# Kernel optimization log

Measured on AMD Instinct MI355X. Metric: run time of the kernel, lower is better.

## Reference

```python
import jax, jax.numpy as jnp
import numpy as np

B, S, D = 1, 2048, 2048
H, KV, HD = 32, 8, 64          # heads, kv heads, head_dim
WINDOW = 1024                  # sliding window (left), causal
ROPE_THETA = 10000.0


def setup_inputs() -> dict:
    key = jax.random.key(0)
    ks = jax.random.split(key, 5)
    scale = 1.0 / np.sqrt(D)
    x = jax.random.normal(ks[0], (B, S, D), dtype=jnp.float32)
    wq = jax.random.normal(ks[1], (D, H * HD), dtype=jnp.float32) * scale
    wk = jax.random.normal(ks[2], (D, KV * HD), dtype=jnp.float32) * scale
    wv = jax.random.normal(ks[3], (D, KV * HD), dtype=jnp.float32) * scale
    wo = jax.random.normal(ks[4], (H * HD, D), dtype=jnp.float32) * scale
    # RoPE frequencies: freqs_cis = exp(i * t * theta^{-2j/hd}), stored as cos/sin
    inv_freq = 1.0 / (ROPE_THETA ** (np.arange(0, HD, 2, dtype=np.float32) / HD))  # [HD/2]
    t = np.arange(S, dtype=np.float32)
    ang = np.outer(t, inv_freq)  # [S, HD/2]
    freqs_cos = jnp.asarray(np.cos(ang), dtype=jnp.float32)
    freqs_sin = jnp.asarray(np.sin(ang), dtype=jnp.float32)
    return {"x": x, "wq": wq, "wk": wk, "wv": wv, "wo": wo,
            "freqs_cos": freqs_cos, "freqs_sin": freqs_sin}


def _apply_rope(t, cos, sin):
    # t: [B,S,h,HD]; pairs (t[...,2i], t[...,2i+1]) form complex numbers
    tr = t.reshape(*t.shape[:-1], HD // 2, 2)
    a, b = tr[..., 0], tr[..., 1]
    c = cos[None, :, None, :]  # [1,S,1,HD/2]
    s = sin[None, :, None, :]
    ra = a * c - b * s
    rb = a * s + b * c
    return jnp.stack([ra, rb], axis=-1).reshape(t.shape)


def reference(x, wq, wk, wv, wo, freqs_cos, freqs_sin):
    q = (x @ wq).reshape(B, S, H, HD)
    k = (x @ wk).reshape(B, S, KV, HD)
    v = (x @ wv).reshape(B, S, KV, HD)
    q = _apply_rope(q, freqs_cos, freqs_sin)
    k = _apply_rope(k, freqs_cos, freqs_sin)
    # GQA: repeat kv heads to match query heads
    k = jnp.repeat(k, H // KV, axis=2)  # [B,S,H,HD]
    v = jnp.repeat(v, H // KV, axis=2)
    scale = jnp.asarray(1.0 / np.sqrt(HD), dtype=x.dtype)
    scores = jnp.einsum('bqhd,bkhd->bhqk', q, k) * scale  # [B,H,S,S]
    i = jnp.arange(S)[:, None]
    j = jnp.arange(S)[None, :]
    allowed = (j <= i) & (j >= i - WINDOW)  # causal + sliding window
    scores = jnp.where(allowed[None, None], scores, jnp.asarray(-1e30, dtype=scores.dtype))
    attn = jax.nn.softmax(scores, axis=-1)
    out = jnp.einsum('bhqk,bkhd->bqhd', attn, v).reshape(B, S, H * HD)
    return out @ wo
```

## Files before the change

### kernel.cpp

```cpp
#include <hip/hip_runtime.h>
#include <stdint.h>

typedef __bf16 bf16_t;
typedef __bf16 bf16x8 __attribute__((ext_vector_type(8)));
typedef __bf16 bf16x4 __attribute__((ext_vector_type(4)));
typedef float floatx4 __attribute__((ext_vector_type(4)));

#define AS3(p) ((__attribute__((address_space(3))) void*)(p))
#define AS1(p) ((__attribute__((address_space(1))) void*)(void*)(p))

__global__ __launch_bounds__(256) void prep_k(const float* __restrict__ x,
                                              const float* __restrict__ wq,
                                              const float* __restrict__ wk,
                                              const float* __restrict__ wv,
                                              const float* __restrict__ wo,
                                              bf16_t* __restrict__ xb,
                                              bf16_t* __restrict__ wt) {
  __shared__ __align__(16) bf16_t T[64][68];
  const int b = blockIdx.x;
  const int t = threadIdx.x;
  if (b < 2048) {
    const int i = (b * 256 + t) * 8;
    floatx4 a = *(const floatx4*)&x[i];
    floatx4 c = *(const floatx4*)&x[i + 4];
    bf16x8 o;
#pragma unroll
    for (int j = 0; j < 4; ++j) { o[j] = (bf16_t)a[j]; o[4 + j] = (bf16_t)c[j]; }
    *(bf16x8*)&xb[i] = o;
    return;
  }
  int b2 = b - 2048;
  const float* src;
  int ncols, bx, by;
  bf16_t* dst;
  if (b2 < 1024) {
    src = wq; ncols = 2048; dst = wt; bx = b2 & 31; by = b2 >> 5;
  } else if (b2 < 1280) {
    const int i2 = b2 - 1024;
    src = wk; ncols = 512; dst = wt + (size_t)2048 * 2048; bx = i2 & 7; by = i2 >> 3;
  } else if (b2 < 1536) {
    const int i2 = b2 - 1280;
    src = wv; ncols = 512; dst = wt + (size_t)2560 * 2048; bx = i2 & 7; by = i2 >> 3;
  } else {
    const int i2 = b2 - 1536;
    src = wo; ncols = 2048; dst = wt + (size_t)3072 * 2048; bx = i2 & 31; by = i2 >> 5;
  }
  const int nt = bx * 64, kt = by * 64;
  const int r0 = t >> 4;
  const int c0 = (t & 15) << 2;
#pragma unroll
  for (int p = 0; p < 4; ++p) {
    const int row = p * 16 + r0;
    floatx4 v = *(const floatx4*)&src[(size_t)(kt + row) * ncols + nt + c0];
    bf16x4 bb;
#pragma unroll
    for (int i = 0; i < 4; ++i) bb[i] = (bf16_t)v[i];
    *(bf16x4*)&T[row][c0] = bb;
  }
  __syncthreads();
#pragma unroll
  for (int p = 0; p < 4; ++p) {
    const int n = p * 16 + r0;
    bf16x4 tmp;
#pragma unroll
    for (int i = 0; i < 4; ++i) tmp[i] = T[c0 + i][n];
    *(bf16x4*)&dst[(size_t)(nt + n) * 2048 + kt + c0] = tmp;
  }
}

template <int EPI>
__global__ __launch_bounds__(256) void gemm_k(const bf16_t* __restrict__ A,
                                              const bf16_t* __restrict__ Bt,
                                              bf16_t* __restrict__ o0,
                                              bf16_t* __restrict__ o1,
                                              bf16_t* __restrict__ o2,
                                              float* __restrict__ fo,
                                              const float* __restrict__ fcos,
                                              const float* __restrict__ fsin) {
  constexpr int K = 2048;
  __shared__ __align__(16) bf16_t As[2][64 * 64];
  __shared__ __align__(16) bf16_t Bs[2][128 * 64];
  const int tid = threadIdx.x;
  const int lane = tid & 63;
  const int w = tid >> 6;
  const int quad = lane >> 4;
  const int l15 = lane & 15;
  const int m0 = blockIdx.y * 64;
  const int n0 = blockIdx.x * 128;
  const int sr = lane >> 3;
  const int sc = ((lane & 7) ^ (sr & 7)) << 3;
  const bf16_t* gA = A + (size_t)(m0 + w * 16 + sr) * K + sc;
  const bf16_t* gB = Bt + (size_t)(n0 + w * 32 + sr) * K + sc;
  floatx4 acc[4][2] = {};

#define GSTAGE(buf, k0)                                                                    \
  do {                                                                                     \
    __builtin_amdgcn_global_load_lds(AS1(gA + (k0)), AS3(&As[buf][w * 1024]), 16, 0, 0);   \
    __builtin_amdgcn_global_load_lds(AS1(gA + 8 * K + (k0)),                               \
                                     AS3(&As[buf][w * 1024 + 512]), 16, 0, 0);             \
    _Pragma("unroll") for (int qq = 0; qq < 4; ++qq)                                       \
        __builtin_amdgcn_global_load_lds(AS1(gB + (size_t)qq * 8 * K + (k0)),              \
                                         AS3(&Bs[buf][w * 2048 + qq * 512]), 16, 0, 0);    \
  } while (0)

#define GCOMPUTE(buf)                                                                      \
  do {                                                                                     \
    _Pragma("unroll") for (int kk = 0; kk < 2; ++kk) {                                     \
      const int co = ((kk * 4 + quad) ^ (l15 & 7)) << 3;                                   \
      bf16x8 af[4], bfr[2];                                                                \
      _Pragma("unroll") for (int i = 0; i < 4; ++i) af[i] =                                \
          *(const bf16x8*)&As[buf][(i * 16 + l15) * 64 + co];                              \
      _Pragma("unroll") for (int i = 0; i < 2; ++i) bfr[i] =                               \
          *(const bf16x8*)&Bs[buf][(w * 32 + i * 16 + l15) * 64 + co];                     \
      _Pragma("unroll") for (int mi = 0; mi < 4; ++mi)                                     \
          _Pragma("unroll") for (int ni = 0; ni < 2; ++ni) acc[mi][ni] =                   \
              __builtin_amdgcn_mfma_f32_16x16x32_bf16(af[mi], bfr[ni], acc[mi][ni], 0, 0,  \
                                                      0);                                  \
    }                                                                                      \
  } while (0)

  GSTAGE(0, 0);
  __syncthreads();
  for (int k0 = 0; k0 < K; k0 += 128) {
    GSTAGE(1, k0 + 64);
    GCOMPUTE(0);
    __syncthreads();
    if (k0 + 128 < K) GSTAGE(0, k0 + 128);
    GCOMPUTE(1);
    __syncthreads();
  }
#undef GSTAGE
#undef GCOMPUTE

  if constexpr (EPI == 0) {
#pragma unroll
    for (int ni = 0; ni < 2; ++ni) {
      const int col = n0 + w * 32 + ni * 16 + l15;
#pragma unroll
      for (int mi = 0; mi < 4; ++mi) {
        const int sb = m0 + mi * 16 + quad * 4;
        if (col < 2560) {
          const int fi = (col & 63) >> 1;
#pragma unroll
          for (int r = 0; r < 4; ++r) {
            const float v = acc[mi][ni][r];
            const float prt = __shfl_xor(v, 1);
            const int s = sb + r;
            const float c = fcos[s * 32 + fi];
            const float sn = fsin[s * 32 + fi];
            const float ov = (col & 1) ? (prt * sn + v * c) : (v * c - prt * sn);
            if (col < 2048)
              o0[(size_t)s * 2048 + col] = (bf16_t)ov;
            else
              o1[(size_t)s * 512 + (col - 2048)] = (bf16_t)ov;
          }
        } else {
          const int sp = (sb & ~31) | (quad * 8 + (mi & 1) * 4);
          bf16x4 pv;
#pragma unroll
          for (int r = 0; r < 4; ++r) pv[r] = (bf16_t)acc[mi][ni][r];
          *(bf16x4*)&o2[(size_t)(col - 2560) * 2048 + sp] = pv;
        }
      }
    }
  } else {
#pragma unroll
    for (int ni = 0; ni < 2; ++ni) {
      const int col = n0 + w * 32 + ni * 16 + l15;
#pragma unroll
      for (int mi = 0; mi < 4; ++mi) {
        const int sb = m0 + mi * 16 + quad * 4;
#pragma unroll
        for (int r = 0; r < 4; ++r) fo[(size_t)(sb + r) * 2048 + col] = acc[mi][ni][r];
      }
    }
  }
}

__global__ __launch_bounds__(256) void attn_k(const bf16_t* __restrict__ qb_,
                                              const bf16_t* __restrict__ kb_,
                                              const bf16_t* __restrict__ vt_,
                                              bf16_t* __restrict__ ob_) {
  __shared__ __align__(16) bf16_t sm[2][8 * 512];
  const int lane = threadIdx.x & 63, w = threadIdx.x >> 6;
  const int quad = lane >> 4, l15 = lane & 15;
  const int h = blockIdx.y, g = h >> 2;
  const int qb = (gridDim.x - 1 - blockIdx.x) * 64;
  const int qw = qb + w * 16;
  const int q = qw + l15;
  const bf16_t* qrow = qb_ + (size_t)q * 2048 + h * 64;
  const bf16x8 qf0 = *(const bf16x8*)(qrow + quad * 8);
  const bf16x8 qf1 = *(const bf16x8*)(qrow + 32 + quad * 8);
  floatx4 acc0 = {}, acc1 = {}, acc2 = {}, acc3 = {}, accl = {};
  const float SC = 0.125f * 1.44269504088896340736f;
  bf16x8 ones;
#pragma unroll
  for (int i = 0; i < 8; ++i) ones[i] = (bf16_t)1.0f;

  int kbB = qb - 1024;
  if (kbB < 0) kbB = 0;
  kbB &= ~31;
  const int nT = (qb + 64 - kbB) >> 5;
  int myS = qw - 1024;
  if (myS < 0) myS = 0;
  myS &= ~31;
  const int myE = qw + 16;

  const int lr = lane & 15, lc = lane >> 4;
  const bf16_t* gk = kb_ + (size_t)(kbB + (w >> 1) * 16 + lr) * 512 + g * 64 +
                     ((w & 1) * 4 + lc) * 8;
  const bf16_t* gv = vt_ + (size_t)(g * 64 + w * 16 + lr) * 2048 + kbB + lc * 8;

#define STAGE(bi, ti)                                                              \
  do {                                                                             \
    __builtin_amdgcn_global_load_lds(AS1(gk + (size_t)(ti) * (32 * 512)),          \
                                     AS3(&sm[bi][w * 512]), 16, 0, 0);             \
    __builtin_amdgcn_global_load_lds(AS1(gv + (size_t)(ti) * 32),                  \
                                     AS3(&sm[bi][(4 + w) * 512]), 16, 0, 0);       \
  } while (0)

#define MSK(pv, key)                                        \
  do {                                                      \
    if ((key) > q || (key) + 1024 < q) pv = -1.0e30f;       \
  } while (0)

  int kb = kbB;
  STAGE(0, 0);
  __syncthreads();
  for (int i = 0; i < nT; ++i, kb += 32) {
    if (i + 1 < nT) STAGE((i + 1) & 1, i + 1);
    if (kb >= myS && kb < myE) {
      const bf16_t* base = &sm[i & 1][(size_t)lane * 8];
      const bf16x8 k0 = *(const bf16x8*)(base);
      const bf16x8 k1 = *(const bf16x8*)(base + 512);
      const bf16x8 k2 = *(const bf16x8*)(base + 1024);
      const bf16x8 k3 = *(const bf16x8*)(base + 1536);
      const bf16x8 v0 = *(const bf16x8*)(base + 2048);
      const bf16x8 v1 = *(const bf16x8*)(base + 2560);
      const bf16x8 v2 = *(const bf16x8*)(base + 3072);
      const bf16x8 v3 = *(const bf16x8*)(base + 3584);
      floatx4 z0 = {}, z1 = {};
      z0 = __builtin_amdgcn_mfma_f32_16x16x32_bf16(k0, qf0, z0, 0, 0, 0);
      z0 = __builtin_amdgcn_mfma_f32_16x16x32_bf16(k1, qf1, z0, 0, 0, 0);
      z1 = __builtin_amdgcn_mfma_f32_16x16x32_bf16(k2, qf0, z1, 0, 0, 0);
      z1 = __builtin_amdgcn_mfma_f32_16x16x32_bf16(k3, qf1, z1, 0, 0, 0);
      float p0 = z0[0] * SC - 32.0f, p1 = z0[1] * SC - 32.0f;
      float p2 = z0[2] * SC - 32.0f, p3 = z0[3] * SC - 32.0f;
      float p4 = z1[0] * SC - 32.0f, p5 = z1[1] * SC - 32.0f;
      float p6 = z1[2] * SC - 32.0f, p7 = z1[3] * SC - 32.0f;
      if ((kb + 31 > qw) || (kb < qw - 1009)) {
        const int kq = kb + quad * 4;
        MSK(p0, kq + 0); MSK(p1, kq + 1); MSK(p2, kq + 2); MSK(p3, kq + 3);
        MSK(p4, kq + 16); MSK(p5, kq + 17); MSK(p6, kq + 18); MSK(p7, kq + 19);
      }
      bf16x8 pf;
      pf[0] = (bf16_t)__builtin_amdgcn_exp2f(p0);
      pf[1] = (bf16_t)__builtin_amdgcn_exp2f(p1);
      pf[2] = (bf16_t)__builtin_amdgcn_exp2f(p2);
      pf[3] = (bf16_t)__builtin_amdgcn_exp2f(p3);
      pf[4] = (bf16_t)__builtin_amdgcn_exp2f(p4);
      pf[5] = (bf16_t)__builtin_amdgcn_exp2f(p5);
      pf[6] = (bf16_t)__builtin_amdgcn_exp2f(p6);
      pf[7] = (bf16_t)__builtin_amdgcn_exp2f(p7);
      accl = __builtin_amdgcn_mfma_f32_16x16x32_bf16(ones, pf, accl, 0, 0, 0);
      acc0 = __builtin_amdgcn_mfma_f32_16x16x32_bf16(v0, pf, acc0, 0, 0, 0);
      acc1 = __builtin_amdgcn_mfma_f32_16x16x32_bf16(v1, pf, acc1, 0, 0, 0);
      acc2 = __builtin_amdgcn_mfma_f32_16x16x32_bf16(v2, pf, acc2, 0, 0, 0);
      acc3 = __builtin_amdgcn_mfma_f32_16x16x32_bf16(v3, pf, acc3, 0, 0, 0);
    }
    __syncthreads();
  }
#undef STAGE
#undef MSK

  const float inv = 1.0f / accl[0];
  bf16_t* obase = ob_ + (size_t)q * 2048 + h * 64 + quad * 4;
  bf16x4 ov;
#pragma unroll
  for (int r = 0; r < 4; ++r) ov[r] = (bf16_t)(acc0[r] * inv);
  *(bf16x4*)(obase) = ov;
#pragma unroll
  for (int r = 0; r < 4; ++r) ov[r] = (bf16_t)(acc1[r] * inv);
  *(bf16x4*)(obase + 16) = ov;
#pragma unroll
  for (int r = 0; r < 4; ++r) ov[r] = (bf16_t)(acc2[r] * inv);
  *(bf16x4*)(obase + 32) = ov;
#pragma unroll
  for (int r = 0; r < 4; ++r) ov[r] = (bf16_t)(acc3[r] * inv);
  *(bf16x4*)(obase + 48) = ov;
}

extern "C" void kernel_launch(void* const* d_in, const int* in_sizes, int n_in, void* d_out,
                              int out_size, void* d_ws, size_t ws_size, hipStream_t stream) {
  (void)in_sizes;
  (void)n_in;
  (void)out_size;
  (void)ws_size;
  const float* x = (const float*)d_in[0];
  const float* wq = (const float*)d_in[1];
  const float* wk = (const float*)d_in[2];
  const float* wv = (const float*)d_in[3];
  const float* wo = (const float*)d_in[4];
  const float* fcos = (const float*)d_in[5];
  const float* fsin = (const float*)d_in[6];
  float* out = (float*)d_out;

  bf16_t* xb = (bf16_t*)d_ws;
  bf16_t* wt = xb + (size_t)2048 * 2048;
  bf16_t* qbuf = wt + (size_t)5120 * 2048;
  bf16_t* kbuf = qbuf + (size_t)2048 * 2048;
  bf16_t* vtb = kbuf + (size_t)2048 * 512;
  bf16_t* att = vtb + (size_t)512 * 2048;

  prep_k<<<4608, 256, 0, stream>>>(x, wq, wk, wv, wo, xb, wt);
  gemm_k<0><<<dim3(24, 32), 256, 0, stream>>>(xb, wt, qbuf, kbuf, vtb, nullptr, fcos, fsin);
  attn_k<<<dim3(32, 32), 256, 0, stream>>>(qbuf, kbuf, vtb, att);
  gemm_k<1><<<dim3(16, 32), 256, 0, stream>>>(att, wt + (size_t)3072 * 2048, nullptr, nullptr,
                                              nullptr, out, fcos, fsin);
}
```

Before: 206.8 us.

## Use 2-warp GEMM blocks with larger per-warp tiles and XCD-aware block remap

Shrinks the GEMM block from 4 to 2 wavefronts. Each wave now computes a 64x64 output tile (4x4 MFMA accumulators) over the same 64x128 block tile, which raises the MFMA-to-LDS-read ratio. Block indices are remapped so that blocks landing on the same XCD work on a contiguous region, to improve L2 reuse. The LDS double buffer is removed in favour of a simple load, sync, compute loop, so global-to-LDS loads no longer overlap with MFMA work. Fewer waves per block also reduces latency hiding.

```diff
diff --git a/kernel.cpp b/kernel.cpp
--- a/kernel.cpp
+++ b/kernel.cpp
@@ -69,7 +69,7 @@
 }
 
 template <int EPI>
-__global__ __launch_bounds__(256) void gemm_k(const bf16_t* __restrict__ A,
+__global__ __launch_bounds__(128) void gemm_k(const bf16_t* __restrict__ A,
                                               const bf16_t* __restrict__ Bt,
                                               bf16_t* __restrict__ o0,
                                               bf16_t* __restrict__ o1,
@@ -78,64 +78,65 @@
                                               const float* __restrict__ fcos,
                                               const float* __restrict__ fsin) {
   constexpr int K = 2048;
-  __shared__ __align__(16) bf16_t As[2][64 * 64];
-  __shared__ __align__(16) bf16_t Bs[2][128 * 64];
+  __shared__ __align__(16) bf16_t As[64 * 64];
+  __shared__ __align__(16) bf16_t Bs[128 * 64];
   const int tid = threadIdx.x;
   const int lane = tid & 63;
   const int w = tid >> 6;
   const int quad = lane >> 4;
   const int l15 = lane & 15;
-  const int m0 = blockIdx.y * 64;
-  const int n0 = blockIdx.x * 128;
+
+  const int nx = gridDim.x, ny = gridDim.y;
+  const int flat = blockIdx.y * nx + blockIdx.x;
+  const int xcd = flat & 7;
+  const int c = flat >> 3;
+  const int CW = nx >> 1, CH = ny >> 2;
+  const int bx = (xcd & 1) * CW + (c % CW);
+  const int by = (xcd >> 1) * CH + (c / CW);
+  const int m0 = by * 64;
+  const int n0 = bx * 128;
+
   const int sr = lane >> 3;
   const int sc = ((lane & 7) ^ (sr & 7)) << 3;
-  const bf16_t* gA = A + (size_t)(m0 + w * 16 + sr) * K + sc;
-  const bf16_t* gB = Bt + (size_t)(n0 + w * 32 + sr) * K + sc;
-  floatx4 acc[4][2] = {};
-
-#define GSTAGE(buf, k0)                                                                    \
-  do {                                                                                     \
-    __builtin_amdgcn_global_load_lds(AS1(gA + (k0)), AS3(&As[buf][w * 1024]), 16, 0, 0);   \
-    __builtin_amdgcn_global_load_lds(AS1(gA + 8 * K + (k0)),                               \
-                                     AS3(&As[buf][w * 1024 + 512]), 16, 0, 0);             \
-    _Pragma("unroll") for (int qq = 0; qq < 4; ++qq)                                       \
-        __builtin_amdgcn_global_load_lds(AS1(gB + (size_t)qq * 8 * K + (k0)),              \
-                                         AS3(&Bs[buf][w * 2048 + qq * 512]), 16, 0, 0);    \
-  } while (0)
-
-#define GCOMPUTE(buf)                                                                      \
-  do {                                                                                     \
-    _Pragma("unroll") for (int kk = 0; kk < 2; ++kk) {                                     \
-      const int co = ((kk * 4 + quad) ^ (l15 & 7)) << 3;                                   \
-      bf16x8 af[4], bfr[2];                                                                \
-      _Pragma("unroll") for (int i = 0; i < 4; ++i) af[i] =                                \
-          *(const bf16x8*)&As[buf][(i * 16 + l15) * 64 + co];                              \
-      _Pragma("unroll") for (int i = 0; i < 2; ++i) bfr[i] =                               \
-          *(const bf16x8*)&Bs[buf][(w * 32 + i * 16 + l15) * 64 + co];                     \
-      _Pragma("unroll") for (int mi = 0; mi < 4; ++mi)                                     \
-          _Pragma("unroll") for (int ni = 0; ni < 2; ++ni) acc[mi][ni] =                   \
-              __builtin_amdgcn_mfma_f32_16x16x32_bf16(af[mi], bfr[ni], acc[mi][ni], 0, 0,  \
-                                                      0);                                  \
-    }                                                                                      \
-  } while (0)
-
-  GSTAGE(0, 0);
-  __syncthreads();
-  for (int k0 = 0; k0 < K; k0 += 128) {
-    GSTAGE(1, k0 + 64);
-    GCOMPUTE(0);
+  const bf16_t* gA = A + (size_t)(m0 + w * 32 + sr) * K + sc;
+  const bf16_t* gB = Bt + (size_t)(n0 + w * 64 + sr) * K + sc;
+  bf16_t* lA = &As[w * 2048];
+  bf16_t* lB = &Bs[w * 4096];
+  floatx4 acc[4][4] = {};
+
+  for (int k0 = 0; k0 < K; k0 += 64) {
+#pragma unroll
+    for (int j = 0; j < 4; ++j)
+      __builtin_amdgcn_global_load_lds(AS1(gA + (size_t)j * 8 * K + k0), AS3(lA + j * 512),
+                                       16, 0, 0);
+#pragma unroll
+    for (int j = 0; j < 8; ++j)
+      __builtin_amdgcn_global_load_lds(AS1(gB + (size_t)j * 8 * K + k0), AS3(lB + j * 512),
+                                       16, 0, 0);
     __syncthreads();
-    if (k0 + 128 < K) GSTAGE(0, k0 + 128);
-    GCOMPUTE(1);
+#pragma unroll
+    for (int kk = 0; kk < 2; ++kk) {
+      const int co = ((kk * 4 + quad) ^ (l15 & 7)) << 3;
+      bf16x8 af[4], bfr[4];
+#pragma unroll
+      for (int i = 0; i < 4; ++i) af[i] = *(const bf16x8*)&As[(i * 16 + l15) * 64 + co];
+#pragma unroll
+      for (int i = 0; i < 4; ++i)
+        bfr[i] = *(const bf16x8*)&Bs[(w * 64 + i * 16 + l15) * 64 + co];
+#pragma unroll
+      for (int mi = 0; mi < 4; ++mi)
+#pragma unroll
+        for (int ni = 0; ni < 4; ++ni)
+          acc[mi][ni] =
+              __builtin_amdgcn_mfma_f32_16x16x32_bf16(af[mi], bfr[ni], acc[mi][ni], 0, 0, 0);
+    }
     __syncthreads();
   }
-#undef GSTAGE
-#undef GCOMPUTE
 
   if constexpr (EPI == 0) {
 #pragma unroll
-    for (int ni = 0; ni < 2; ++ni) {
-      const int col = n0 + w * 32 + ni * 16 + l15;
+    for (int ni = 0; ni < 4; ++ni) {
+      const int col = n0 + w * 64 + ni * 16 + l15;
 #pragma unroll
       for (int mi = 0; mi < 4; ++mi) {
         const int sb = m0 + mi * 16 + quad * 4;
@@ -146,9 +147,9 @@
             const float v = acc[mi][ni][r];
             const float prt = __shfl_xor(v, 1);
             const int s = sb + r;
-            const float c = fcos[s * 32 + fi];
+            const float cc = fcos[s * 32 + fi];
             const float sn = fsin[s * 32 + fi];
-            const float ov = (col & 1) ? (prt * sn + v * c) : (v * c - prt * sn);
+            const float ov = (col & 1) ? (prt * sn + v * cc) : (v * cc - prt * sn);
             if (col < 2048)
               o0[(size_t)s * 2048 + col] = (bf16_t)ov;
             else
@@ -165,8 +166,8 @@
     }
   } else {
 #pragma unroll
-    for (int ni = 0; ni < 2; ++ni) {
-      const int col = n0 + w * 32 + ni * 16 + l15;
+    for (int ni = 0; ni < 4; ++ni) {
+      const int col = n0 + w * 64 + ni * 16 + l15;
 #pragma unroll
       for (int mi = 0; mi < 4; ++mi) {
         const int sb = m0 + mi * 16 + quad * 4;
@@ -313,8 +314,8 @@
   bf16_t* att = vtb + (size_t)512 * 2048;
 
   prep_k<<<4608, 256, 0, stream>>>(x, wq, wk, wv, wo, xb, wt);
-  gemm_k<0><<<dim3(24, 32), 256, 0, stream>>>(xb, wt, qbuf, kbuf, vtb, nullptr, fcos, fsin);
+  gemm_k<0><<<dim3(24, 32), 128, 0, stream>>>(xb, wt, qbuf, kbuf, vtb, nullptr, fcos, fsin);
   attn_k<<<dim3(32, 32), 256, 0, stream>>>(qbuf, kbuf, vtb, att);
-  gemm_k<1><<<dim3(16, 32), 256, 0, stream>>>(att, wt + (size_t)3072 * 2048, nullptr, nullptr,
+  gemm_k<1><<<dim3(16, 32), 128, 0, stream>>>(att, wt + (size_t)3072 * 2048, nullptr, nullptr,
                                               nullptr, out, fcos, fsin);
 }
```

New measurement: 232.9 us. 1.13x slower.

## Replace full syncthreads with partial vmcnt waits and remap GEMM blocks per XCD

Applied to the files above, without the earlier changes.

In the GEMM and attention loops, each __syncthreads (which waits for all outstanding memory ops) is replaced by explicit s_waitcnt vmcnt(N)/lgkmcnt(0) plus s_barrier. This lets the next stage's async global-to-LDS loads stay in flight while the current buffer is consumed. The GEMM also remaps flat block IDs so blocks on the same XCD work on a contiguous tile region, aiming for better L2 reuse. The remap assumes the grid divides evenly (nx by 2, ny by 4), and the attention loop now issues a redundant final stage load to keep vmcnt counts uniform.

```diff
diff --git a/kernel.cpp b/kernel.cpp
--- a/kernel.cpp
+++ b/kernel.cpp
@@ -85,52 +85,73 @@
   const int w = tid >> 6;
   const int quad = lane >> 4;
   const int l15 = lane & 15;
-  const int m0 = blockIdx.y * 64;
-  const int n0 = blockIdx.x * 128;
+
+  const int nx = gridDim.x, ny = gridDim.y;
+  const int flat = blockIdx.y * nx + blockIdx.x;
+  const int xcd = flat & 7;
+  const int c = flat >> 3;
+  const int CW = nx >> 1, CH = ny >> 2;
+  const int bx = (xcd & 1) * CW + (c % CW);
+  const int by = (xcd >> 1) * CH + (c / CW);
+  const int m0 = by * 64;
+  const int n0 = bx * 128;
+
   const int sr = lane >> 3;
   const int sc = ((lane & 7) ^ (sr & 7)) << 3;
   const bf16_t* gA = A + (size_t)(m0 + w * 16 + sr) * K + sc;
   const bf16_t* gB = Bt + (size_t)(n0 + w * 32 + sr) * K + sc;
   floatx4 acc[4][2] = {};
 
-#define GSTAGE(buf, k0)                                                                    \
-  do {                                                                                     \
-    __builtin_amdgcn_global_load_lds(AS1(gA + (k0)), AS3(&As[buf][w * 1024]), 16, 0, 0);   \
-    __builtin_amdgcn_global_load_lds(AS1(gA + 8 * K + (k0)),                               \
-                                     AS3(&As[buf][w * 1024 + 512]), 16, 0, 0);             \
-    _Pragma("unroll") for (int qq = 0; qq < 4; ++qq)                                       \
-        __builtin_amdgcn_global_load_lds(AS1(gB + (size_t)qq * 8 * K + (k0)),              \
-                                         AS3(&Bs[buf][w * 2048 + qq * 512]), 16, 0, 0);    \
+#define GSTAGE(buf, k0)                                                                  \
+  do {                                                                                   \
+    __builtin_amdgcn_global_load_lds(AS1(gA + (k0)), AS3(&As[buf][w * 1024]), 16, 0, 0); \
+    __builtin_amdgcn_global_load_lds(AS1(gA + 8 * K + (k0)),                             \
+                                     AS3(&As[buf][w * 1024 + 512]), 16, 0, 0);           \
+    _Pragma("unroll") for (int qq = 0; qq < 4; ++qq)                                     \
+        __builtin_amdgcn_global_load_lds(AS1(gB + (size_t)qq * 8 * K + (k0)),            \
+                                         AS3(&Bs[buf][w * 2048 + qq * 512]), 16, 0, 0);  \
   } while (0)
 
-#define GCOMPUTE(buf)                                                                      \
-  do {                                                                                     \
-    _Pragma("unroll") for (int kk = 0; kk < 2; ++kk) {                                     \
-      const int co = ((kk * 4 + quad) ^ (l15 & 7)) << 3;                                   \
-      bf16x8 af[4], bfr[2];                                                                \
-      _Pragma("unroll") for (int i = 0; i < 4; ++i) af[i] =                                \
-          *(const bf16x8*)&As[buf][(i * 16 + l15) * 64 + co];                              \
-      _Pragma("unroll") for (int i = 0; i < 2; ++i) bfr[i] =                               \
-          *(const bf16x8*)&Bs[buf][(w * 32 + i * 16 + l15) * 64 + co];                     \
-      _Pragma("unroll") for (int mi = 0; mi < 4; ++mi)                                     \
-          _Pragma("unroll") for (int ni = 0; ni < 2; ++ni) acc[mi][ni] =                   \
-              __builtin_amdgcn_mfma_f32_16x16x32_bf16(af[mi], bfr[ni], acc[mi][ni], 0, 0,  \
-                                                      0);                                  \
-    }                                                                                      \
+#define GCOMP(buf)                                                                       \
+  do {                                                                                   \
+    _Pragma("unroll") for (int kk = 0; kk < 2; ++kk) {                                   \
+      const int co = ((kk * 4 + quad) ^ (l15 & 7)) << 3;                                 \
+      bf16x8 af[4], bfr[2];                                                              \
+      _Pragma("unroll") for (int i = 0; i < 4; ++i) af[i] =                              \
+          *(const bf16x8*)&As[buf][(i * 16 + l15) * 64 + co];                            \
+      _Pragma("unroll") for (int i = 0; i < 2; ++i) bfr[i] =                             \
+          *(const bf16x8*)&Bs[buf][(w * 32 + i * 16 + l15) * 64 + co];                   \
+      _Pragma("unroll") for (int mi = 0; mi < 4; ++mi)                                   \
+          _Pragma("unroll") for (int ni = 0; ni < 2; ++ni) acc[mi][ni] =                 \
+              __builtin_amdgcn_mfma_f32_16x16x32_bf16(af[mi], bfr[ni], acc[mi][ni], 0,   \
+                                                      0, 0);                             \
+    }                                                                                    \
   } while (0)
 
   GSTAGE(0, 0);
-  __syncthreads();
-  for (int k0 = 0; k0 < K; k0 += 128) {
+  for (int k0 = 0; k0 < K - 128; k0 += 128) {
     GSTAGE(1, k0 + 64);
-    GCOMPUTE(0);
-    __syncthreads();
-    if (k0 + 128 < K) GSTAGE(0, k0 + 128);
-    GCOMPUTE(1);
-    __syncthreads();
-  }
+    asm volatile("s_waitcnt vmcnt(6)" ::: "memory");
+    __builtin_amdgcn_s_barrier();
+    GCOMP(0);
+    asm volatile("s_waitcnt lgkmcnt(0)" ::: "memory");
+    __builtin_amdgcn_s_barrier();
+    GSTAGE(0, k0 + 128);
+    asm volatile("s_waitcnt vmcnt(6)" ::: "memory");
+    __builtin_amdgcn_s_barrier();
+    GCOMP(1);
+    asm volatile("s_waitcnt lgkmcnt(0)" ::: "memory");
+    __builtin_amdgcn_s_barrier();
+  }
+  GSTAGE(1, K - 64);
+  asm volatile("s_waitcnt vmcnt(6)" ::: "memory");
+  __builtin_amdgcn_s_barrier();
+  GCOMP(0);
+  asm volatile("s_waitcnt vmcnt(0) lgkmcnt(0)" ::: "memory");
+  __builtin_amdgcn_s_barrier();
+  GCOMP(1);
 #undef GSTAGE
-#undef GCOMPUTE
+#undef GCOMP
 
   if constexpr (EPI == 0) {
 #pragma unroll
@@ -146,9 +167,9 @@
             const float v = acc[mi][ni][r];
             const float prt = __shfl_xor(v, 1);
             const int s = sb + r;
-            const float c = fcos[s * 32 + fi];
+            const float cc = fcos[s * 32 + fi];
             const float sn = fsin[s * 32 + fi];
-            const float ov = (col & 1) ? (prt * sn + v * c) : (v * c - prt * sn);
+            const float ov = (col & 1) ? (prt * sn + v * cc) : (v * cc - prt * sn);
             if (col < 2048)
               o0[(size_t)s * 2048 + col] = (bf16_t)ov;
             else
@@ -226,9 +247,11 @@
 
   int kb = kbB;
   STAGE(0, 0);
-  __syncthreads();
   for (int i = 0; i < nT; ++i, kb += 32) {
-    if (i + 1 < nT) STAGE((i + 1) & 1, i + 1);
+    const int ti = (i + 1 < nT) ? i + 1 : i;
+    STAGE((i + 1) & 1, ti);
+    asm volatile("s_waitcnt vmcnt(2)" ::: "memory");
+    __builtin_amdgcn_s_barrier();
     if (kb >= myS && kb < myE) {
       const bf16_t* base = &sm[i & 1][(size_t)lane * 8];
       const bf16x8 k0 = *(const bf16x8*)(base);
@@ -268,7 +291,8 @@
       acc2 = __builtin_amdgcn_mfma_f32_16x16x32_bf16(v2, pf, acc2, 0, 0, 0);
       acc3 = __builtin_amdgcn_mfma_f32_16x16x32_bf16(v3, pf, acc3, 0, 0, 0);
     }
-    __syncthreads();
+    asm volatile("s_waitcnt lgkmcnt(0)" ::: "memory");
+    __builtin_amdgcn_s_barrier();
   }
 #undef STAGE
 #undef MSK
```

Result: no change. 207.4 us (+0.3%).
